# Optimization experiments

Measured on AMD Instinct MI355X. Metric: run time of the kernel, lower is better.

Reference implementation:

```python
import jax, jax.numpy as jnp
import numpy as np

B, S, D = 2, 2048, 2048
H, KV, HD = 16, 8, 128
N_REP = H // KV


def _rotate_half(x):
    x1, x2 = x[..., : x.shape[-1] // 2], x[..., x.shape[-1] // 2 :]
    return jnp.concatenate((-x2, x1), axis=-1)


def setup_inputs() -> dict:
    key = jax.random.key(0)
    ks = jax.random.split(key, 5)
    x = jax.random.normal(ks[0], (B, S, D), dtype=jnp.float32)
    # rotary tables (llama-style): inv_freq over half dims, duplicated
    inv_freq = 1.0 / (10000.0 ** (jnp.arange(0, HD, 2, dtype=jnp.float32) / HD))
    t = jnp.arange(S, dtype=jnp.float32)
    freqs = jnp.outer(t, inv_freq)                      # [S, HD/2]
    emb = jnp.concatenate((freqs, freqs), axis=-1)      # [S, HD]
    cos, sin = jnp.cos(emb), jnp.sin(emb)
    sc = 0.02
    Wq = jax.random.normal(ks[1], (D, H * HD), dtype=jnp.float32) * sc
    Wk = jax.random.normal(ks[2], (D, KV * HD), dtype=jnp.float32) * sc
    Wv = jax.random.normal(ks[3], (D, KV * HD), dtype=jnp.float32) * sc
    Wo = jax.random.normal(ks[4], (H * HD, D), dtype=jnp.float32) * sc
    return {"x": x, "cos": cos, "sin": sin, "Wq": Wq, "Wk": Wk, "Wv": Wv, "Wo": Wo}


def reference(x, cos, sin, Wq, Wk, Wv, Wo):
    b, s, _ = x.shape
    q = (x @ Wq).reshape(b, s, H, HD)
    k = (x @ Wk).reshape(b, s, KV, HD)
    v = (x @ Wv).reshape(b, s, KV, HD)
    # RoPE (broadcast over batch and heads; unsqueeze_dim=2 layout [b,s,h,d])
    c = cos[None, :, None, :]
    sn = sin[None, :, None, :]
    q = q * c + _rotate_half(q) * sn
    k = k * c + _rotate_half(k) * sn
    # GQA expansion (repeat_kv == interleaved repeat along head dim)
    k = jnp.repeat(k, N_REP, axis=2)
    v = jnp.repeat(v, N_REP, axis=2)
    scale = HD ** -0.5
    # causal attention (single-rank ring attention == one causal flash block)
    scores = jnp.einsum("bqhd,bkhd->bhqk", q, k) * scale
    mask = jnp.tril(jnp.ones((s, s), dtype=bool))
    scores = jnp.where(mask[None, None], scores, -jnp.inf)
    probs = jax.nn.softmax(scores, axis=-1)
    attn = jnp.einsum("bhqk,bkhd->bqhd", probs, v).reshape(b, s, H * HD)
    return attn @ Wo
```

## Files before the change

kernel.cpp:

```cpp
#include <hip/hip_runtime.h>


typedef __bf16 bf16;
typedef __bf16 bf16x4 __attribute__((ext_vector_type(4)));
typedef __bf16 bf16x8 __attribute__((ext_vector_type(8)));
typedef float floatx4 __attribute__((ext_vector_type(4)));

#define AS1(p) ((const __attribute__((address_space(1))) void*)(p))
#define AS3(p) ((__attribute__((address_space(3))) void*)(p))

__device__ __forceinline__ void load16(const void* g, void* l) {
  __builtin_amdgcn_global_load_lds(AS1(g), AS3(l), 16, 0, 0);
}

__device__ __forceinline__ void phase_barrier() {
  asm volatile("" ::: "memory");
  __builtin_amdgcn_sched_barrier(0);
  __builtin_amdgcn_s_barrier();
  __builtin_amdgcn_sched_barrier(0);
  asm volatile("" ::: "memory");
}

__global__ __launch_bounds__(256) void prep_kernel(
    const float* __restrict__ x, const float* __restrict__ Wq,
    const float* __restrict__ Wk, const float* __restrict__ Wv,
    const float* __restrict__ Wo, bf16* __restrict__ xb,
    bf16* __restrict__ WqkvT, bf16* __restrict__ WoT) {
  __shared__ float tile[32][33];
  const int bi = blockIdx.x;
  if (bi < 8192) {
    int i = bi * 256 + threadIdx.x;
    float4 v = ((const float4*)x)[i];
    bf16x4 o = {(bf16)v.x, (bf16)v.y, (bf16)v.z, (bf16)v.w};
    ((bf16x4*)xb)[i] = o;
    return;
  }
  const int i2 = bi - 8192;
  const int wid = i2 >> 12;
  const int r0 = ((i2 >> 6) & 63) * 32;
  const int c0 = (i2 & 63) * 32;
  const float* src = wid == 0 ? Wq : wid == 1 ? Wk : wid == 2 ? Wv : Wo;
  bf16* dst = wid == 0 ? WqkvT
            : wid == 1 ? WqkvT + 2048ull * 2048
            : wid == 2 ? WqkvT + 3072ull * 2048
                       : WoT;
  const int ncols = (wid == 1 || wid == 2) ? 1024 : 2048;
  if (c0 >= ncols) return;
  const int tx = threadIdx.x & 31, ty = threadIdx.x >> 5;
#pragma unroll
  for (int i = 0; i < 4; i++) {
    int ri = ty + i * 8;
    tile[ri][tx] = src[(long)(r0 + ri) * ncols + c0 + tx];
  }
  __syncthreads();
#pragma unroll
  for (int i = 0; i < 4; i++) {
    int ci = ty + i * 8;
    dst[(long)(c0 + ci) * 2048 + r0 + tx] = (bf16)tile[tx][ci];
  }
}

__global__ __launch_bounds__(256) void mid_kernel(
    bf16* __restrict__ QKV, const float* __restrict__ cosb,
    const float* __restrict__ sinb, bf16* __restrict__ Vtb) {
  __shared__ bf16 tile[32][33];
  const int bi = blockIdx.x;
  if (bi < 24576) {
    int idx = bi * 256 + threadIdx.x;
    int nh, nhs, offc;
    if (idx < 4194304) { nh = 16; nhs = 4; offc = 0; }
    else { idx -= 4194304; nh = 8; nhs = 3; offc = 2048; }
    int d = idx & 63;
    int rest = idx >> 6;
    int hh = rest & (nh - 1);
    int bs = rest >> nhs;
    int s = bs & 2047;
    size_t base = (size_t)bs * 4096 + offc + hh * 128;
    float c0 = cosb[s * 128 + d];
    float c1 = cosb[s * 128 + d + 64];
    float s0 = sinb[s * 128 + d];
    float s1 = sinb[s * 128 + d + 64];
    float x0 = (float)QKV[base + d];
    float x1 = (float)QKV[base + d + 64];
    QKV[base + d] = (bf16)(x0 * c0 - x1 * s0);
    QKV[base + d + 64] = (bf16)(x1 * c1 + x0 * s1);
    return;
  }
  const int i2 = bi - 24576;
  const int z = i2 >> 11;
  const int r0 = ((i2 >> 5) & 63) * 32;
  const int c0 = (i2 & 31) * 32;
  const bf16* in = QKV + 3072;
  const long ib = 2048ll * 4096 * z, ob = 1024ll * 2048 * z;
  const int tx = threadIdx.x & 31, ty = threadIdx.x >> 5;
#pragma unroll
  for (int i = 0; i < 4; i++) {
    int ri = ty + i * 8;
    tile[ri][tx] = in[ib + (long)(r0 + ri) * 4096 + c0 + tx];
  }
  __syncthreads();
#pragma unroll
  for (int i = 0; i < 4; i++) {
    int ci = ty + i * 8;
    Vtb[ob + (long)(c0 + ci) * 2048 + r0 + tx] = tile[tx][ci];
  }
}

template <typename CT>
__global__ __launch_bounds__(512, 2) void gemm256(
    const bf16* __restrict__ A, const bf16* __restrict__ Bt, CT* __restrict__ C,
    int M, int N, int K) {
  __shared__ __align__(1024) char smem[131072];
  const int tid = threadIdx.x;
  const int wave = tid >> 6, lane = tid & 63;
  const int quad = lane >> 4, l16 = lane & 15;
  const int wm = wave >> 2, wn = wave & 3;
  const int m0 = blockIdx.y * 256, n0 = blockIdx.x * 256;

  const int srow = (wave >> 1) * 16 + (lane >> 2);
  const int skcol = (wave & 1) * 32 + (((lane & 3) * 8) ^ ((lane & 32) ? 16 : 0));
  const int sblk = wave * 1024;

  const int qoff = (quad * 16) ^ ((l16 & 8) << 2);
  const int aoff = wm * 16384 + l16 * 64 + qoff;
  const int boff = 32768 + (wn >> 1) * 16384 + (wn & 1) * 8192 + l16 * 64 + qoff;

  auto stageA = [&](int kt, int h, int buf) {
    const bf16* g = A + (size_t)(m0 + h * 128 + srow) * K + kt * 64 + skcol;
    char* d = smem + buf * 65536 + h * 16384 + sblk;
    load16(g, d);
    load16(g + (size_t)64 * K, d + 8192);
  };
  auto stageB = [&](int kt, int h, int buf) {
    const bf16* g = Bt + (size_t)(n0 + h * 128 + srow) * K + kt * 64 + skcol;
    char* d = smem + buf * 65536 + 32768 + h * 16384 + sblk;
    load16(g, d);
    load16(g + (size_t)64 * K, d + 8192);
  };
  auto rdA = [&](int buf, int fr, int ks) {
    return *(const bf16x8*)(smem + buf * 65536 + aoff + (fr * 2 + ks) * 1024);
  };
  auto rdB = [&](int buf, int fc, int ks) {
    return *(const bf16x8*)(smem + buf * 65536 + boff + (fc * 2 + ks) * 1024);
  };

  floatx4 acc[8][4] = {};

  const int nkt = K >> 6;
  const int niter = nkt >> 1;

  stageB(0, 0, 0); stageB(0, 1, 0);
  stageA(0, 0, 0); stageA(0, 1, 0);
  stageB(1, 0, 1); stageB(1, 1, 1);
  asm volatile("s_waitcnt vmcnt(4)" ::: "memory");
  phase_barrier();

  for (int it = 0; it < niter; ++it) {
    const int T = 2 * it;
    const bool morek = (it < niter - 1);
#pragma unroll
    for (int c = 0; c < 2; ++c) {
      const int buf = c;
      const int tA = T + 1 + c;
      const int tB = T + 2 + c;
      const bool stA = (c == 0) || morek;

      bf16x8 a[4][2], b01[2][2], b23[2][2];

#pragma unroll
      for (int fr = 0; fr < 4; ++fr)
#pragma unroll
        for (int ks = 0; ks < 2; ++ks) a[fr][ks] = rdA(buf, fr, ks);
#pragma unroll
      for (int fc = 0; fc < 2; ++fc)
#pragma unroll
        for (int ks = 0; ks < 2; ++ks) b01[fc][ks] = rdB(buf, fc, ks);
      if (stA) stageA(tA, 0, buf ^ 1);
      phase_barrier();
      __builtin_amdgcn_s_setprio(1);
#pragma unroll
      for (int ks = 0; ks < 2; ++ks)
#pragma unroll
        for (int fr = 0; fr < 4; ++fr)
#pragma unroll
          for (int fc = 0; fc < 2; ++fc)
            acc[fr][fc] = __builtin_amdgcn_mfma_f32_16x16x32_bf16(
                a[fr][ks], b01[fc][ks], acc[fr][fc], 0, 0, 0);
      __builtin_amdgcn_s_setprio(0);
      phase_barrier();

#pragma unroll
      for (int fc = 0; fc < 2; ++fc)
#pragma unroll
        for (int ks = 0; ks < 2; ++ks) b23[fc][ks] = rdB(buf, 2 + fc, ks);
      if (stA) stageA(tA, 1, buf ^ 1);
      phase_barrier();
      __builtin_amdgcn_s_setprio(1);
#pragma unroll
      for (int ks = 0; ks < 2; ++ks)
#pragma unroll
        for (int fr = 0; fr < 4; ++fr)
#pragma unroll
          for (int fc = 0; fc < 2; ++fc)
            acc[fr][2 + fc] = __builtin_amdgcn_mfma_f32_16x16x32_bf16(
                a[fr][ks], b23[fc][ks], acc[fr][2 + fc], 0, 0, 0);
      __builtin_amdgcn_s_setprio(0);
      phase_barrier();

#pragma unroll
      for (int fr = 0; fr < 4; ++fr)
#pragma unroll
        for (int ks = 0; ks < 2; ++ks) a[fr][ks] = rdA(buf, 4 + fr, ks);
      if (morek) stageB(tB, 0, buf);
      phase_barrier();
      __builtin_amdgcn_s_setprio(1);
#pragma unroll
      for (int ks = 0; ks < 2; ++ks)
#pragma unroll
        for (int fr = 0; fr < 4; ++fr)
#pragma unroll
          for (int fc = 0; fc < 2; ++fc)
            acc[4 + fr][2 + fc] = __builtin_amdgcn_mfma_f32_16x16x32_bf16(
                a[fr][ks], b23[fc][ks], acc[4 + fr][2 + fc], 0, 0, 0);
      __builtin_amdgcn_s_setprio(0);
      phase_barrier();

      if (morek) stageB(tB, 1, buf);
      if (morek)
        asm volatile("s_waitcnt vmcnt(4)" ::: "memory");
      else
        asm volatile("s_waitcnt vmcnt(0)" ::: "memory");
      phase_barrier();
      __builtin_amdgcn_s_setprio(1);
#pragma unroll
      for (int ks = 0; ks < 2; ++ks)
#pragma unroll
        for (int fr = 0; fr < 4; ++fr)
#pragma unroll
          for (int fc = 0; fc < 2; ++fc)
            acc[4 + fr][fc] = __builtin_amdgcn_mfma_f32_16x16x32_bf16(
                a[fr][ks], b01[fc][ks], acc[4 + fr][fc], 0, 0, 0);
      __builtin_amdgcn_s_setprio(0);
      phase_barrier();
    }
  }

#pragma unroll
  for (int fr = 0; fr < 8; ++fr)
#pragma unroll
    for (int fc = 0; fc < 4; ++fc)
#pragma unroll
      for (int r = 0; r < 4; ++r) {
        int row = m0 + wm * 128 + fr * 16 + quad * 4 + r;
        int col = n0 + wn * 64 + fc * 16 + l16;
        C[(size_t)row * N + col] = (CT)acc[fr][fc][r];
      }
}

__global__ __launch_bounds__(512, 1) void gemm256x128(
    const bf16* __restrict__ A, const bf16* __restrict__ Bt, float* __restrict__ C,
    int M, int N, int K) {
  __shared__ __align__(1024) char smem[98304];
  const int tid = threadIdx.x;
  const int wave = tid >> 6, lane = tid & 63;
  const int quad = lane >> 4, l16 = lane & 15;
  const int wm = wave >> 1, wn = wave & 1;
  const int m0 = blockIdx.y * 256, n0 = blockIdx.x * 128;

  const int srow = (wave >> 1) * 16 + (lane >> 2);
  const int skcol = (wave & 1) * 32 + (((lane & 3) * 8) ^ ((lane & 32) ? 16 : 0));
  const int sblk = wave * 1024;

  const int qoff = (quad * 16) ^ ((l16 & 8) << 2);
  const int aoff = (wm >> 1) * 16384 + l16 * 64 + qoff;
  const int afrag = (wm & 1) * 4;
  const int boff = 32768 + l16 * 64 + qoff;
  const int bfrag = wn * 4;

  auto stageA = [&](int kt, int h, int buf) {
    const bf16* g = A + (size_t)(m0 + h * 128 + srow) * K + kt * 64 + skcol;
    char* d = smem + buf * 49152 + h * 16384 + sblk;
    load16(g, d);
    load16(g + (size_t)64 * K, d + 8192);
  };
  auto stageB = [&](int kt, int buf) {
    const bf16* g = Bt + (size_t)(n0 + srow) * K + kt * 64 + skcol;
    char* d = smem + buf * 49152 + 32768 + sblk;
    load16(g, d);
    load16(g + (size_t)64 * K, d + 8192);
  };
  auto rdA = [&](int buf, int fr, int ks) {
    return *(const bf16x8*)(smem + buf * 49152 + aoff + ((afrag + fr) * 2 + ks) * 1024);
  };
  auto rdB = [&](int buf, int fc, int ks) {
    return *(const bf16x8*)(smem + buf * 49152 + boff + ((bfrag + fc) * 2 + ks) * 1024);
  };

  floatx4 acc[4][4] = {};

  const int nkt = K >> 6;
  const int niter = nkt >> 1;

  stageB(0, 0);
  stageA(0, 0, 0); stageA(0, 1, 0);
  stageB(1, 1);
  asm volatile("s_waitcnt vmcnt(2)" ::: "memory");
  phase_barrier();

  for (int it = 0; it < niter; ++it) {
    const int T = 2 * it;
    const bool morek = (it < niter - 1);
#pragma unroll
    for (int c = 0; c < 2; ++c) {
      const int buf = c;
      const int tA = T + 1 + c;
      const int tB = T + 2 + c;
      const bool stA = (c == 0) || morek;

      bf16x8 a[2][2], b01[2][2], b23[2][2];

#pragma unroll
      for (int fr = 0; fr < 2; ++fr)
#pragma unroll
        for (int ks = 0; ks < 2; ++ks) a[fr][ks] = rdA(buf, fr, ks);
#pragma unroll
      for (int fc = 0; fc < 2; ++fc)
#pragma unroll
        for (int ks = 0; ks < 2; ++ks) b01[fc][ks] = rdB(buf, fc, ks);
      if (stA) stageA(tA, 0, buf ^ 1);
      phase_barrier();
      __builtin_amdgcn_s_setprio(1);
#pragma unroll
      for (int ks = 0; ks < 2; ++ks)
#pragma unroll
        for (int fr = 0; fr < 2; ++fr)
#pragma unroll
          for (int fc = 0; fc < 2; ++fc)
            acc[fr][fc] = __builtin_amdgcn_mfma_f32_16x16x32_bf16(
                a[fr][ks], b01[fc][ks], acc[fr][fc], 0, 0, 0);
      __builtin_amdgcn_s_setprio(0);
      phase_barrier();

#pragma unroll
      for (int fc = 0; fc < 2; ++fc)
#pragma unroll
        for (int ks = 0; ks < 2; ++ks) b23[fc][ks] = rdB(buf, 2 + fc, ks);
      if (stA) stageA(tA, 1, buf ^ 1);
      phase_barrier();
      __builtin_amdgcn_s_setprio(1);
#pragma unroll
      for (int ks = 0; ks < 2; ++ks)
#pragma unroll
        for (int fr = 0; fr < 2; ++fr)
#pragma unroll
          for (int fc = 0; fc < 2; ++fc)
            acc[fr][2 + fc] = __builtin_amdgcn_mfma_f32_16x16x32_bf16(
                a[fr][ks], b23[fc][ks], acc[fr][2 + fc], 0, 0, 0);
      __builtin_amdgcn_s_setprio(0);
      phase_barrier();

#pragma unroll
      for (int fr = 0; fr < 2; ++fr)
#pragma unroll
        for (int ks = 0; ks < 2; ++ks) a[fr][ks] = rdA(buf, 2 + fr, ks);
      if (morek) stageB(tB, buf);
      phase_barrier();
      __builtin_amdgcn_s_setprio(1);
#pragma unroll
      for (int ks = 0; ks < 2; ++ks)
#pragma unroll
        for (int fr = 0; fr < 2; ++fr)
#pragma unroll
          for (int fc = 0; fc < 2; ++fc)
            acc[2 + fr][2 + fc] = __builtin_amdgcn_mfma_f32_16x16x32_bf16(
                a[fr][ks], b23[fc][ks], acc[2 + fr][2 + fc], 0, 0, 0);
      __builtin_amdgcn_s_setprio(0);
      phase_barrier();

      if (morek)
        asm volatile("s_waitcnt vmcnt(2)" ::: "memory");
      else
        asm volatile("s_waitcnt vmcnt(0)" ::: "memory");
      phase_barrier();
      __builtin_amdgcn_s_setprio(1);
#pragma unroll
      for (int ks = 0; ks < 2; ++ks)
#pragma unroll
        for (int fr = 0; fr < 2; ++fr)
#pragma unroll
          for (int fc = 0; fc < 2; ++fc)
            acc[2 + fr][fc] = __builtin_amdgcn_mfma_f32_16x16x32_bf16(
                a[fr][ks], b01[fc][ks], acc[2 + fr][fc], 0, 0, 0);
      __builtin_amdgcn_s_setprio(0);
      phase_barrier();
    }
  }

#pragma unroll
  for (int fr = 0; fr < 4; ++fr)
#pragma unroll
    for (int fc = 0; fc < 4; ++fc)
#pragma unroll
      for (int r = 0; r < 4; ++r) {
        int row = m0 + wm * 64 + fr * 16 + quad * 4 + r;
        int col = n0 + wn * 64 + fc * 16 + l16;
        C[(size_t)row * N + col] = acc[fr][fc][r];
      }
}


template <bool MASK>
__device__ __forceinline__ void attn_step32(
    const bf16* Kc, const bf16* Vc, bf16* Pw, const bf16x8 (&aq)[4],
    const bf16x8& ones, floatx4 (&oacc)[8], floatx4& lacc,
    int k0, int q0w, int l16, int quad) {
  floatx4 sacc[4] = {};
  __builtin_amdgcn_s_setprio(1);
#pragma unroll
  for (int ks = 0; ks < 4; ks++)
#pragma unroll
    for (int j = 0; j < 4; j++) {
      int row = j * 16 + l16;
      bf16x8 bk = *(const bf16x8*)(Kc + row * 128 + (((ks * 4 + quad) ^ (row & 15)) * 8));
      sacc[j] = __builtin_amdgcn_mfma_f32_16x16x32_bf16(aq[ks], bk, sacc[j], 0, 0, 0);
    }
  __builtin_amdgcn_s_setprio(0);
  const float C = 0.12752188659023044f;
#pragma unroll
  for (int r = 0; r < 4; r++) {
    int row = quad * 4 + r;
#pragma unroll
    for (int j = 0; j < 4; j++) {
      float p = exp2f(sacc[j][r] * C);
      if (MASK) {
        int key = k0 + j * 16 + l16;
        if (key > q0w + row) p = 0.f;
      }
      int col = j * 16 + l16;
      Pw[row * 64 + (((col >> 3) ^ (row & 7)) * 8) + (col & 7)] = (bf16)p;
    }
  }
  __builtin_amdgcn_s_setprio(1);
#pragma unroll
  for (int ks = 0; ks < 2; ks++) {
    bf16x8 ap = *(const bf16x8*)(Pw + l16 * 64 + (((ks * 4 + quad) ^ (l16 & 7)) * 8));
    lacc = __builtin_amdgcn_mfma_f32_16x16x32_bf16(ap, ones, lacc, 0, 0, 0);
#pragma unroll
    for (int j = 0; j < 8; j++) {
      int vr = j * 16 + l16;
      bf16x8 bv = *(const bf16x8*)(Vc + vr * 64 + (((ks * 4 + quad) ^ (vr & 7)) * 8));
      oacc[j] = __builtin_amdgcn_mfma_f32_16x16x32_bf16(ap, bv, oacc[j], 0, 0, 0);
    }
  }
  __builtin_amdgcn_s_setprio(0);
}

__global__ __launch_bounds__(512, 4) void flash_kernel(
    const bf16* __restrict__ QKV, const bf16* __restrict__ Vt, bf16* __restrict__ O) {
  __shared__ __align__(1024) char smem[81920];
  const int tid = threadIdx.x;
  const int wave = tid >> 6, lane = tid & 63, quad = lane >> 4, l16 = lane & 15;
  const int wbase = tid & ~63;
  const int hloc = wave & 1, rgroup = wave >> 1;
  bf16* Pw = (bf16*)(smem + 65536) + wave * 1024;
  bf16x8 ones;
#pragma unroll
  for (int e = 0; e < 8; e++) ones[e] = (bf16)1.0f;

  const int w = blockIdx.x;
  const int side = w & 1, kvh = (w >> 1) & 7, b = (w >> 4) & 1, g = w >> 5;
  const int p = (g < 8) ? (2 * g + side) : (31 - 2 * (g - 8) - side);
  const int qt = (((kvh >> 2) ^ b) & 1) ? 31 - p : p;
  const int h = kvh * 2 + hloc;
  const int q0 = qt * 64;
  const int nkt = qt + 1;

#pragma unroll
  for (int u = 0; u < 4; u++) {
    int gg = u * 512 + tid;
    int row = gg >> 4, cc = gg & 15;
    const bf16* gp = QKV + (size_t)(b * 2048 + q0 + (row & 63)) * 4096 +
                     (kvh * 2 + (row >> 6)) * 128 + ((cc ^ (row & 15)) * 8);
    load16(gp, smem + (u * 512 + wbase) * 16);
  }
  asm volatile("s_waitcnt vmcnt(0)" ::: "memory");
  phase_barrier();
  bf16x8 aq[4];
  {
    int qr = hloc * 64 + rgroup * 16 + l16;
#pragma unroll
    for (int ks = 0; ks < 4; ks++)
      aq[ks] = *(const bf16x8*)((const bf16*)smem + qr * 128 +
                                (((ks * 4 + quad) ^ (qr & 15)) * 8));
  }
  __syncthreads();

  auto stageKV = [&](int kt, int nb) {
    char* kd = smem + nb * 16384;
    char* vd = smem + 32768 + nb * 16384;
#pragma unroll
    for (int u = 0; u < 2; u++) {
      int gg = u * 512 + tid;
      int krow = gg >> 4, kcc = gg & 15;
      const bf16* kp = QKV + (size_t)(b * 2048 + kt * 64 + krow) * 4096 + 2048 +
                       kvh * 128 + ((kcc ^ (krow & 15)) * 8);
      load16(kp, kd + (u * 512 + wbase) * 16);
      int vrow = gg >> 3, vcc = gg & 7;
      const bf16* vp = Vt + (size_t)(b * 1024 + kvh * 128 + vrow) * 2048 + kt * 64 +
                       ((vcc ^ (vrow & 7)) * 8);
      load16(vp, vd + (u * 512 + wbase) * 16);
    }
  };

  stageKV(0, 0);

  floatx4 oacc[8] = {};
  floatx4 lacc = {};
  const int q0w = q0 + rgroup * 16;

  for (int kt = 0; kt < nkt; kt++) {
    const int cur = kt & 1;
    if (kt + 1 < nkt) {
      stageKV(kt + 1, cur ^ 1);
      asm volatile("s_waitcnt vmcnt(4)" ::: "memory");
    } else {
      asm volatile("s_waitcnt vmcnt(0)" ::: "memory");
    }
    phase_barrier();
    const bf16* Kc = (const bf16*)(smem + cur * 16384);
    const bf16* Vc = (const bf16*)(smem + 32768 + cur * 16384);
    if (kt == nkt - 1)
      attn_step32<true>(Kc, Vc, Pw, aq, ones, oacc, lacc, kt * 64, q0w, l16, quad);
    else
      attn_step32<false>(Kc, Vc, Pw, aq, ones, oacc, lacc, kt * 64, q0w, l16, quad);
    phase_barrier();
  }

  float rl[4];
#pragma unroll
  for (int r = 0; r < 4; r++) rl[r] = 1.0f / lacc[r];
#pragma unroll
  for (int j = 0; j < 8; j++)
#pragma unroll
    for (int r = 0; r < 4; r++) {
      int s = q0w + quad * 4 + r;
      O[(size_t)(b * 2048 + s) * 2048 + h * 128 + j * 16 + l16] =
          (bf16)(oacc[j][r] * rl[r]);
    }
}

extern "C" void kernel_launch(void* const* d_in, const int* in_sizes, int n_in,
                              void* d_out, int out_size, void* d_ws, size_t ws_size,
                              hipStream_t stream) {
  (void)in_sizes; (void)n_in; (void)out_size; (void)ws_size;
  const float* x    = (const float*)d_in[0];
  const float* cosb = (const float*)d_in[1];
  const float* sinb = (const float*)d_in[2];
  const float* Wq   = (const float*)d_in[3];
  const float* Wk   = (const float*)d_in[4];
  const float* Wv   = (const float*)d_in[5];
  const float* Wo   = (const float*)d_in[6];
  float* out = (float*)d_out;

  char* ws = (char*)d_ws;
  size_t off = 0;
  auto alloc = [&](size_t bytes) { void* p = ws + off; off += bytes; return p; };
  bf16* xb    = (bf16*)alloc(4096ull * 2048 * 2);
  bf16* WqkvT = (bf16*)alloc(4096ull * 2048 * 2);
  bf16* WoT   = (bf16*)alloc(2048ull * 2048 * 2);
  bf16* QKV   = (bf16*)alloc(4096ull * 4096 * 2);
  bf16* Vtb   = (bf16*)alloc(2048ull * 2048 * 2);
  bf16* Ab    = (bf16*)alloc(4096ull * 2048 * 2);

  prep_kernel<<<8192 + 16384, 256, 0, stream>>>(x, Wq, Wk, Wv, Wo, xb, WqkvT, WoT);

  gemm256<bf16><<<dim3(16, 16), 512, 0, stream>>>(xb, WqkvT, QKV, 4096, 4096, 2048);

  mid_kernel<<<24576 + 4096, 256, 0, stream>>>(QKV, cosb, sinb, Vtb);

  flash_kernel<<<dim3(512, 1, 1), 512, 0, stream>>>(QKV, Vtb, Ab);

  gemm256x128<<<dim3(16, 16), 512, 0, stream>>>(Ab, WoT, out, 4096, 2048, 2048);
}
```

Measured before the change: 298.9 us.

## Convert QKV GEMM to single-buffered LDS with in-place quarter-tile refills

The 256x256 QKV projection GEMM now uses one 64 KB LDS buffer instead of two 64 KB stages. The next K-tile's A and B quarters are loaded into the same buffer as soon as each quarter's fragments have been read into registers. This halves shared-memory use and raises the launch-bounds occupancy hint. The risk is exposed load latency, since each refill must land before the next iteration with less lookahead than double buffering provides. The grid of 256 blocks is too small for higher occupancy to help much.

```diff
diff --git a/kernel.cpp b/kernel.cpp
--- a/kernel.cpp
+++ b/kernel.cpp
@@ -107,10 +107,10 @@
 }
 
 template <typename CT>
-__global__ __launch_bounds__(512, 2) void gemm256(
+__global__ __launch_bounds__(512, 4) void gemm256sb(
     const bf16* __restrict__ A, const bf16* __restrict__ Bt, CT* __restrict__ C,
     int M, int N, int K) {
-  __shared__ __align__(1024) char smem[131072];
+  __shared__ __align__(1024) char smem[65536];
   const int tid = threadIdx.x;
   const int wave = tid >> 6, lane = tid & 63;
   const int quad = lane >> 4, l16 = lane & 15;
@@ -123,126 +123,115 @@
 
   const int qoff = (quad * 16) ^ ((l16 & 8) << 2);
   const int aoff = wm * 16384 + l16 * 64 + qoff;
-  const int boff = 32768 + (wn >> 1) * 16384 + (wn & 1) * 8192 + l16 * 64 + qoff;
-
-  auto stageA = [&](int kt, int h, int buf) {
-    const bf16* g = A + (size_t)(m0 + h * 128 + srow) * K + kt * 64 + skcol;
-    char* d = smem + buf * 65536 + h * 16384 + sblk;
-    load16(g, d);
-    load16(g + (size_t)64 * K, d + 8192);
-  };
-  auto stageB = [&](int kt, int h, int buf) {
-    const bf16* g = Bt + (size_t)(n0 + h * 128 + srow) * K + kt * 64 + skcol;
-    char* d = smem + buf * 65536 + 32768 + h * 16384 + sblk;
-    load16(g, d);
-    load16(g + (size_t)64 * K, d + 8192);
-  };
-  auto rdA = [&](int buf, int fr, int ks) {
-    return *(const bf16x8*)(smem + buf * 65536 + aoff + (fr * 2 + ks) * 1024);
-  };
-  auto rdB = [&](int buf, int fc, int ks) {
-    return *(const bf16x8*)(smem + buf * 65536 + boff + (fc * 2 + ks) * 1024);
+  const int boff = 32768 + wn * 8192 + l16 * 64 + qoff;
+
+  auto stageAq = [&](int kt, int q) {
+    const bf16* g = A + (size_t)(m0 + q * 64 + srow) * K + kt * 64 + skcol;
+    load16(g, smem + q * 8192 + sblk);
+  };
+  auto stageBr = [&](int kt, int r) {
+    const bf16* g = Bt + (size_t)(n0 + r * 64 + srow) * K + kt * 64 + skcol;
+    load16(g, smem + 32768 + r * 8192 + sblk);
+  };
+  auto rdA = [&](int fr, int ks) {
+    return *(const bf16x8*)(smem + aoff + (fr * 2 + ks) * 1024);
+  };
+  auto rdB = [&](int fc, int ks) {
+    return *(const bf16x8*)(smem + boff + (fc * 2 + ks) * 1024);
   };
 
   floatx4 acc[8][4] = {};
-
   const int nkt = K >> 6;
-  const int niter = nkt >> 1;
-
-  stageB(0, 0, 0); stageB(0, 1, 0);
-  stageA(0, 0, 0); stageA(0, 1, 0);
-  stageB(1, 0, 1); stageB(1, 1, 1);
-  asm volatile("s_waitcnt vmcnt(4)" ::: "memory");
+
+  stageAq(0, 0); stageAq(0, 2);
+  stageBr(0, 0); stageBr(0, 1); stageBr(0, 2); stageBr(0, 3);
+  stageAq(0, 1); stageAq(0, 3);
+  asm volatile("s_waitcnt vmcnt(2)" ::: "memory");
   phase_barrier();
 
-  for (int it = 0; it < niter; ++it) {
-    const int T = 2 * it;
-    const bool morek = (it < niter - 1);
-#pragma unroll
-    for (int c = 0; c < 2; ++c) {
-      const int buf = c;
-      const int tA = T + 1 + c;
-      const int tB = T + 2 + c;
-      const bool stA = (c == 0) || morek;
-
-      bf16x8 a[4][2], b01[2][2], b23[2][2];
-
+  for (int t = 0; t < nkt; ++t) {
+    const bool morek = (t + 1 < nkt);
+    bf16x8 a[4][2], b01[2][2], b23[2][2];
+
+#pragma unroll
+    for (int fr = 0; fr < 4; ++fr)
+#pragma unroll
+      for (int ks = 0; ks < 2; ++ks) a[fr][ks] = rdA(fr, ks);
+#pragma unroll
+    for (int fc = 0; fc < 2; ++fc)
+#pragma unroll
+      for (int ks = 0; ks < 2; ++ks) b01[fc][ks] = rdB(fc, ks);
+    phase_barrier();
+    __builtin_amdgcn_s_setprio(1);
+#pragma unroll
+    for (int ks = 0; ks < 2; ++ks)
 #pragma unroll
       for (int fr = 0; fr < 4; ++fr)
 #pragma unroll
-        for (int ks = 0; ks < 2; ++ks) a[fr][ks] = rdA(buf, fr, ks);
-#pragma unroll
-      for (int fc = 0; fc < 2; ++fc)
-#pragma unroll
-        for (int ks = 0; ks < 2; ++ks) b01[fc][ks] = rdB(buf, fc, ks);
-      if (stA) stageA(tA, 0, buf ^ 1);
-      phase_barrier();
-      __builtin_amdgcn_s_setprio(1);
-#pragma unroll
-      for (int ks = 0; ks < 2; ++ks)
-#pragma unroll
-        for (int fr = 0; fr < 4; ++fr)
-#pragma unroll
-          for (int fc = 0; fc < 2; ++fc)
-            acc[fr][fc] = __builtin_amdgcn_mfma_f32_16x16x32_bf16(
-                a[fr][ks], b01[fc][ks], acc[fr][fc], 0, 0, 0);
-      __builtin_amdgcn_s_setprio(0);
-      phase_barrier();
-
-#pragma unroll
-      for (int fc = 0; fc < 2; ++fc)
-#pragma unroll
-        for (int ks = 0; ks < 2; ++ks) b23[fc][ks] = rdB(buf, 2 + fc, ks);
-      if (stA) stageA(tA, 1, buf ^ 1);
-      phase_barrier();
-      __builtin_amdgcn_s_setprio(1);
-#pragma unroll
-      for (int ks = 0; ks < 2; ++ks)
-#pragma unroll
-        for (int fr = 0; fr < 4; ++fr)
-#pragma unroll
-          for (int fc = 0; fc < 2; ++fc)
-            acc[fr][2 + fc] = __builtin_amdgcn_mfma_f32_16x16x32_bf16(
-                a[fr][ks], b23[fc][ks], acc[fr][2 + fc], 0, 0, 0);
-      __builtin_amdgcn_s_setprio(0);
-      phase_barrier();
-
+        for (int fc = 0; fc < 2; ++fc)
+          acc[fr][fc] = __builtin_amdgcn_mfma_f32_16x16x32_bf16(
+              a[fr][ks], b01[fc][ks], acc[fr][fc], 0, 0, 0);
+    __builtin_amdgcn_s_setprio(0);
+    phase_barrier();
+
+#pragma unroll
+    for (int fc = 0; fc < 2; ++fc)
+#pragma unroll
+      for (int ks = 0; ks < 2; ++ks) b23[fc][ks] = rdB(2 + fc, ks);
+    if (morek) { stageAq(t + 1, 0); stageAq(t + 1, 2); }
+    if (morek)
+      asm volatile("s_waitcnt vmcnt(2)" ::: "memory");
+    else
+      asm volatile("s_waitcnt vmcnt(0)" ::: "memory");
+    phase_barrier();
+    __builtin_amdgcn_s_setprio(1);
+#pragma unroll
+    for (int ks = 0; ks < 2; ++ks)
 #pragma unroll
       for (int fr = 0; fr < 4; ++fr)
 #pragma unroll
-        for (int ks = 0; ks < 2; ++ks) a[fr][ks] = rdA(buf, 4 + fr, ks);
-      if (morek) stageB(tB, 0, buf);
-      phase_barrier();
-      __builtin_amdgcn_s_setprio(1);
-#pragma unroll
-      for (int ks = 0; ks < 2; ++ks)
-#pragma unroll
-        for (int fr = 0; fr < 4; ++fr)
-#pragma unroll
-          for (int fc = 0; fc < 2; ++fc)
-            acc[4 + fr][2 + fc] = __builtin_amdgcn_mfma_f32_16x16x32_bf16(
-                a[fr][ks], b23[fc][ks], acc[4 + fr][2 + fc], 0, 0, 0);
-      __builtin_amdgcn_s_setprio(0);
-      phase_barrier();
-
-      if (morek) stageB(tB, 1, buf);
-      if (morek)
-        asm volatile("s_waitcnt vmcnt(4)" ::: "memory");
-      else
-        asm volatile("s_waitcnt vmcnt(0)" ::: "memory");
-      phase_barrier();
-      __builtin_amdgcn_s_setprio(1);
-#pragma unroll
-      for (int ks = 0; ks < 2; ++ks)
-#pragma unroll
-        for (int fr = 0; fr < 4; ++fr)
-#pragma unroll
-          for (int fc = 0; fc < 2; ++fc)
-            acc[4 + fr][fc] = __builtin_amdgcn_mfma_f32_16x16x32_bf16(
-                a[fr][ks], b01[fc][ks], acc[4 + fr][fc], 0, 0, 0);
-      __builtin_amdgcn_s_setprio(0);
-      phase_barrier();
-    }
+        for (int fc = 0; fc < 2; ++fc)
+          acc[fr][2 + fc] = __builtin_amdgcn_mfma_f32_16x16x32_bf16(
+              a[fr][ks], b23[fc][ks], acc[fr][2 + fc], 0, 0, 0);
+    __builtin_amdgcn_s_setprio(0);
+    phase_barrier();
+
+#pragma unroll
+    for (int fr = 0; fr < 4; ++fr)
+#pragma unroll
+      for (int ks = 0; ks < 2; ++ks) a[fr][ks] = rdA(4 + fr, ks);
+    if (morek) {
+      stageBr(t + 1, 0); stageBr(t + 1, 1); stageBr(t + 1, 2); stageBr(t + 1, 3);
+    }
+    phase_barrier();
+    __builtin_amdgcn_s_setprio(1);
+#pragma unroll
+    for (int ks = 0; ks < 2; ++ks)
+#pragma unroll
+      for (int fr = 0; fr < 4; ++fr)
+#pragma unroll
+        for (int fc = 0; fc < 2; ++fc)
+          acc[4 + fr][2 + fc] = __builtin_amdgcn_mfma_f32_16x16x32_bf16(
+              a[fr][ks], b23[fc][ks], acc[4 + fr][2 + fc], 0, 0, 0);
+    __builtin_amdgcn_s_setprio(0);
+    phase_barrier();
+
+    if (morek) {
+      stageAq(t + 1, 1); stageAq(t + 1, 3);
+      asm volatile("s_waitcnt vmcnt(2)" ::: "memory");
+    }
+    phase_barrier();
+    __builtin_amdgcn_s_setprio(1);
+#pragma unroll
+    for (int ks = 0; ks < 2; ++ks)
+#pragma unroll
+      for (int fr = 0; fr < 4; ++fr)
+#pragma unroll
+        for (int fc = 0; fc < 2; ++fc)
+          acc[4 + fr][fc] = __builtin_amdgcn_mfma_f32_16x16x32_bf16(
+              a[fr][ks], b01[fc][ks], acc[4 + fr][fc], 0, 0, 0);
+    __builtin_amdgcn_s_setprio(0);
+    phase_barrier();
   }
 
 #pragma unroll
@@ -407,7 +396,6 @@
         C[(size_t)row * N + col] = acc[fr][fc][r];
       }
 }
-
 
 template <bool MASK>
 __device__ __forceinline__ void attn_step32(
@@ -574,7 +562,7 @@
 
   prep_kernel<<<8192 + 16384, 256, 0, stream>>>(x, Wq, Wk, Wv, Wo, xb, WqkvT, WoT);
 
-  gemm256<bf16><<<dim3(16, 16), 512, 0, stream>>>(xb, WqkvT, QKV, 4096, 4096, 2048);
+  gemm256sb<bf16><<<dim3(16, 16), 512, 0, stream>>>(xb, WqkvT, QKV, 4096, 4096, 2048);
 
   mid_kernel<<<24576 + 4096, 256, 0, stream>>>(QKV, cosb, sinb, Vtb);
 
```

New measurement: 801.5 us. 168% more time.

## Triple-buffer A tiles in QKV GEMM to prefetch two k-steps ahead

Applied to the files above, without the earlier changes.

Reworks the QKV projection GEMM's shared-memory pipeline. A tiles now use three LDS buffers and B tiles two, and every global load is issued two k-tiles ahead through a single flat loop instead of the old two-way unrolled double-buffer scheme. The aim is to hide more global-load latency behind the MFMA phases. In exchange LDS use grows from 128 KB to 160 KB per block, which could limit the two-blocks-per-CU occupancy the launch bounds ask for, and the kt%3 indexing adds some address arithmetic.

```diff
diff --git a/kernel.cpp b/kernel.cpp
--- a/kernel.cpp
+++ b/kernel.cpp
@@ -107,10 +107,10 @@
 }
 
 template <typename CT>
-__global__ __launch_bounds__(512, 2) void gemm256(
+__global__ __launch_bounds__(512, 2) void gemm256ta(
     const bf16* __restrict__ A, const bf16* __restrict__ Bt, CT* __restrict__ C,
     int M, int N, int K) {
-  __shared__ __align__(1024) char smem[131072];
+  __shared__ __align__(1024) char smem[163840];
   const int tid = threadIdx.x;
   const int wave = tid >> 6, lane = tid & 63;
   const int quad = lane >> 4, l16 = lane & 15;
@@ -123,126 +123,117 @@
 
   const int qoff = (quad * 16) ^ ((l16 & 8) << 2);
   const int aoff = wm * 16384 + l16 * 64 + qoff;
-  const int boff = 32768 + (wn >> 1) * 16384 + (wn & 1) * 8192 + l16 * 64 + qoff;
-
-  auto stageA = [&](int kt, int h, int buf) {
+  const int boff = 98304 + (wn >> 1) * 16384 + (wn & 1) * 8192 + l16 * 64 + qoff;
+
+  auto stageA = [&](int kt, int h) {
     const bf16* g = A + (size_t)(m0 + h * 128 + srow) * K + kt * 64 + skcol;
-    char* d = smem + buf * 65536 + h * 16384 + sblk;
+    char* d = smem + (kt % 3) * 32768 + h * 16384 + sblk;
     load16(g, d);
     load16(g + (size_t)64 * K, d + 8192);
   };
-  auto stageB = [&](int kt, int h, int buf) {
+  auto stageB = [&](int kt, int h) {
     const bf16* g = Bt + (size_t)(n0 + h * 128 + srow) * K + kt * 64 + skcol;
-    char* d = smem + buf * 65536 + 32768 + h * 16384 + sblk;
+    char* d = smem + 98304 + (kt & 1) * 32768 + h * 16384 + sblk;
     load16(g, d);
     load16(g + (size_t)64 * K, d + 8192);
   };
-  auto rdA = [&](int buf, int fr, int ks) {
-    return *(const bf16x8*)(smem + buf * 65536 + aoff + (fr * 2 + ks) * 1024);
-  };
-  auto rdB = [&](int buf, int fc, int ks) {
-    return *(const bf16x8*)(smem + buf * 65536 + boff + (fc * 2 + ks) * 1024);
+  auto rdA = [&](int am, int fr, int ks) {
+    return *(const bf16x8*)(smem + am + aoff + (fr * 2 + ks) * 1024);
+  };
+  auto rdB = [&](int bc, int fc, int ks) {
+    return *(const bf16x8*)(smem + bc + boff + (fc * 2 + ks) * 1024);
   };
 
   floatx4 acc[8][4] = {};
-
   const int nkt = K >> 6;
-  const int niter = nkt >> 1;
-
-  stageB(0, 0, 0); stageB(0, 1, 0);
-  stageA(0, 0, 0); stageA(0, 1, 0);
-  stageB(1, 0, 1); stageB(1, 1, 1);
-  asm volatile("s_waitcnt vmcnt(4)" ::: "memory");
+
+  stageA(0, 0); stageA(0, 1); stageB(0, 0); stageB(0, 1);
+  stageA(1, 0); stageA(1, 1); stageB(1, 0); stageB(1, 1);
+  asm volatile("s_waitcnt vmcnt(8)" ::: "memory");
   phase_barrier();
 
-  for (int it = 0; it < niter; ++it) {
-    const int T = 2 * it;
-    const bool morek = (it < niter - 1);
-#pragma unroll
-    for (int c = 0; c < 2; ++c) {
-      const int buf = c;
-      const int tA = T + 1 + c;
-      const int tB = T + 2 + c;
-      const bool stA = (c == 0) || morek;
-
-      bf16x8 a[4][2], b01[2][2], b23[2][2];
-
+  for (int t = 0; t < nkt; ++t) {
+    const bool st2 = (t + 2 < nkt);
+    const int am = (t % 3) * 32768;
+    const int bc = (t & 1) * 32768;
+    bf16x8 a[4][2], b01[2][2], b23[2][2];
+
+#pragma unroll
+    for (int fr = 0; fr < 4; ++fr)
+#pragma unroll
+      for (int ks = 0; ks < 2; ++ks) a[fr][ks] = rdA(am, fr, ks);
+#pragma unroll
+    for (int fc = 0; fc < 2; ++fc)
+#pragma unroll
+      for (int ks = 0; ks < 2; ++ks) b01[fc][ks] = rdB(bc, fc, ks);
+    if (st2) stageA(t + 2, 0);
+    phase_barrier();
+    __builtin_amdgcn_s_setprio(1);
+#pragma unroll
+    for (int ks = 0; ks < 2; ++ks)
 #pragma unroll
       for (int fr = 0; fr < 4; ++fr)
 #pragma unroll
-        for (int ks = 0; ks < 2; ++ks) a[fr][ks] = rdA(buf, fr, ks);
-#pragma unroll
-      for (int fc = 0; fc < 2; ++fc)
-#pragma unroll
-        for (int ks = 0; ks < 2; ++ks) b01[fc][ks] = rdB(buf, fc, ks);
-      if (stA) stageA(tA, 0, buf ^ 1);
-      phase_barrier();
-      __builtin_amdgcn_s_setprio(1);
-#pragma unroll
-      for (int ks = 0; ks < 2; ++ks)
-#pragma unroll
-        for (int fr = 0; fr < 4; ++fr)
-#pragma unroll
-          for (int fc = 0; fc < 2; ++fc)
-            acc[fr][fc] = __builtin_amdgcn_mfma_f32_16x16x32_bf16(
-                a[fr][ks], b01[fc][ks], acc[fr][fc], 0, 0, 0);
-      __builtin_amdgcn_s_setprio(0);
-      phase_barrier();
-
-#pragma unroll
-      for (int fc = 0; fc < 2; ++fc)
-#pragma unroll
-        for (int ks = 0; ks < 2; ++ks) b23[fc][ks] = rdB(buf, 2 + fc, ks);
-      if (stA) stageA(tA, 1, buf ^ 1);
-      phase_barrier();
-      __builtin_amdgcn_s_setprio(1);
-#pragma unroll
-      for (int ks = 0; ks < 2; ++ks)
-#pragma unroll
-        for (int fr = 0; fr < 4; ++fr)
-#pragma unroll
-          for (int fc = 0; fc < 2; ++fc)
-            acc[fr][2 + fc] = __builtin_amdgcn_mfma_f32_16x16x32_bf16(
-                a[fr][ks], b23[fc][ks], acc[fr][2 + fc], 0, 0, 0);
-      __builtin_amdgcn_s_setprio(0);
-      phase_barrier();
-
+        for (int fc = 0; fc < 2; ++fc)
+          acc[fr][fc] = __builtin_amdgcn_mfma_f32_16x16x32_bf16(
+              a[fr][ks], b01[fc][ks], acc[fr][fc], 0, 0, 0);
+    __builtin_amdgcn_s_setprio(0);
+    phase_barrier();
+
+#pragma unroll
+    for (int fc = 0; fc < 2; ++fc)
+#pragma unroll
+      for (int ks = 0; ks < 2; ++ks) b23[fc][ks] = rdB(bc, 2 + fc, ks);
+    if (st2) stageA(t + 2, 1);
+    phase_barrier();
+    __builtin_amdgcn_s_setprio(1);
+#pragma unroll
+    for (int ks = 0; ks < 2; ++ks)
 #pragma unroll
       for (int fr = 0; fr < 4; ++fr)
 #pragma unroll
-        for (int ks = 0; ks < 2; ++ks) a[fr][ks] = rdA(buf, 4 + fr, ks);
-      if (morek) stageB(tB, 0, buf);
-      phase_barrier();
-      __builtin_amdgcn_s_setprio(1);
-#pragma unroll
-      for (int ks = 0; ks < 2; ++ks)
-#pragma unroll
-        for (int fr = 0; fr < 4; ++fr)
-#pragma unroll
-          for (int fc = 0; fc < 2; ++fc)
-            acc[4 + fr][2 + fc] = __builtin_amdgcn_mfma_f32_16x16x32_bf16(
-                a[fr][ks], b23[fc][ks], acc[4 + fr][2 + fc], 0, 0, 0);
-      __builtin_amdgcn_s_setprio(0);
-      phase_barrier();
-
-      if (morek) stageB(tB, 1, buf);
-      if (morek)
-        asm volatile("s_waitcnt vmcnt(4)" ::: "memory");
-      else
-        asm volatile("s_waitcnt vmcnt(0)" ::: "memory");
-      phase_barrier();
-      __builtin_amdgcn_s_setprio(1);
-#pragma unroll
-      for (int ks = 0; ks < 2; ++ks)
-#pragma unroll
-        for (int fr = 0; fr < 4; ++fr)
-#pragma unroll
-          for (int fc = 0; fc < 2; ++fc)
-            acc[4 + fr][fc] = __builtin_amdgcn_mfma_f32_16x16x32_bf16(
-                a[fr][ks], b01[fc][ks], acc[4 + fr][fc], 0, 0, 0);
-      __builtin_amdgcn_s_setprio(0);
-      phase_barrier();
-    }
+        for (int fc = 0; fc < 2; ++fc)
+          acc[fr][2 + fc] = __builtin_amdgcn_mfma_f32_16x16x32_bf16(
+              a[fr][ks], b23[fc][ks], acc[fr][2 + fc], 0, 0, 0);
+    __builtin_amdgcn_s_setprio(0);
+    phase_barrier();
+
+#pragma unroll
+    for (int fr = 0; fr < 4; ++fr)
+#pragma unroll
+      for (int ks = 0; ks < 2; ++ks) a[fr][ks] = rdA(am, 4 + fr, ks);
+    if (st2) stageB(t + 2, 0);
+    phase_barrier();
+    __builtin_amdgcn_s_setprio(1);
+#pragma unroll
+    for (int ks = 0; ks < 2; ++ks)
+#pragma unroll
+      for (int fr = 0; fr < 4; ++fr)
+#pragma unroll
+        for (int fc = 0; fc < 2; ++fc)
+          acc[4 + fr][2 + fc] = __builtin_amdgcn_mfma_f32_16x16x32_bf16(
+              a[fr][ks], b23[fc][ks], acc[4 + fr][2 + fc], 0, 0, 0);
+    __builtin_amdgcn_s_setprio(0);
+    phase_barrier();
+
+    if (st2) {
+      stageB(t + 2, 1);
+      asm volatile("s_waitcnt vmcnt(8)" ::: "memory");
+    } else {
+      asm volatile("s_waitcnt vmcnt(0)" ::: "memory");
+    }
+    phase_barrier();
+    __builtin_amdgcn_s_setprio(1);
+#pragma unroll
+    for (int ks = 0; ks < 2; ++ks)
+#pragma unroll
+      for (int fr = 0; fr < 4; ++fr)
+#pragma unroll
+        for (int fc = 0; fc < 2; ++fc)
+          acc[4 + fr][fc] = __builtin_amdgcn_mfma_f32_16x16x32_bf16(
+              a[fr][ks], b01[fc][ks], acc[4 + fr][fc], 0, 0, 0);
+    __builtin_amdgcn_s_setprio(0);
+    phase_barrier();
   }
 
 #pragma unroll
@@ -407,7 +398,6 @@
         C[(size_t)row * N + col] = acc[fr][fc][r];
       }
 }
-
 
 template <bool MASK>
 __device__ __forceinline__ void attn_step32(
@@ -574,7 +564,7 @@
 
   prep_kernel<<<8192 + 16384, 256, 0, stream>>>(x, Wq, Wk, Wv, Wo, xb, WqkvT, WoT);
 
-  gemm256<bf16><<<dim3(16, 16), 512, 0, stream>>>(xb, WqkvT, QKV, 4096, 4096, 2048);
+  gemm256ta<bf16><<<dim3(16, 16), 512, 0, stream>>>(xb, WqkvT, QKV, 4096, 4096, 2048);
 
   mid_kernel<<<24576 + 4096, 256, 0, stream>>>(QKV, cosb, sinb, Vtb);
 
```

Result: slower. 305.1 us (+2.1%).
